# Optimization experiments

Hardware: AMD Instinct MI355X
Metric: run time of the kernel (lower is better)

Reference implementation:

```python
import jax, jax.numpy as jnp
import numpy as np

N_NODES = 100000


def mean_aggregate(x, src, dst, n_nodes):
    # gather messages from src nodes, mean-reduce onto dst nodes (DGL copy_u + mean)
    msg = x[src]                                                  # [E, d]
    summed = jax.ops.segment_sum(msg, dst, num_segments=n_nodes)  # [N, d]
    cnt = jax.ops.segment_sum(jnp.ones((src.shape[0],), x.dtype), dst,
                              num_segments=n_nodes)               # [N]
    # zero in-degree nodes get mean 0 (matches DGL mean reducer)
    return summed / jnp.maximum(cnt, 1.0)[:, None]


def setup_inputs() -> dict:
    key = jax.random.key(0)
    ks = jax.random.split(key, 7)
    E = 1600000
    d_in, d_hid, d_out = 128, 128, 128
    features = jax.random.normal(ks[0], (N_NODES, d_in), dtype=jnp.float32)
    src = jax.random.randint(ks[1], (E,), 0, N_NODES, dtype=jnp.int64)
    dst = jax.random.randint(ks[2], (E,), 0, N_NODES, dtype=jnp.int64)
    W1 = jax.random.normal(ks[3], (d_hid, d_in), dtype=jnp.float32) * (1.0 / np.sqrt(d_in))
    b1 = jax.random.normal(ks[4], (d_hid,), dtype=jnp.float32) * 0.01
    W2 = jax.random.normal(ks[5], (d_out, d_hid), dtype=jnp.float32) * (1.0 / np.sqrt(d_hid))
    b2 = jax.random.normal(ks[6], (d_out,), dtype=jnp.float32) * 0.01
    return {"features": features, "src": src, "dst": dst,
            "W1": W1, "b1": b1, "W2": W2, "b2": b2}


def reference(features, src, dst, W1, b1, W2, b2):
    # GINConv (eps=0, mean agg): h = Linear((1+eps)*x + mean_neigh(x))
    agg1 = mean_aggregate(features, src, dst, N_NODES)
    x1 = jax.nn.relu(jnp.dot(features + agg1, W1.T) + b1)   # layer1 + outer relu
    agg2 = mean_aggregate(x1, src, dst, N_NODES)
    x2 = jnp.dot(x1 + agg2, W2.T) + b2                       # layer2, no activation
    return x2
```

## Files before the change

kernel.cpp:

```cpp
#include <hip/hip_runtime.h>

#define D 128
#define CAP_A 12288
#define BIN_SHIFT 9
#define FRAG_CAP 80
#define NBLK_A 256

typedef __attribute__((ext_vector_type(8))) short bf16x8;
typedef __attribute__((ext_vector_type(4))) float f32x4;

static __device__ __forceinline__ unsigned short f2bf(float f) {
    unsigned int u = __float_as_uint(f);
    unsigned int r = (u + 0x7fffu + ((u >> 16) & 1u)) >> 16;
    return (unsigned short)r;
}
static __device__ __forceinline__ float bf2f(unsigned short u) {
    return __uint_as_float((unsigned int)u << 16);
}

__global__ void f2bf_kernel(const float4* __restrict__ in, ushort4* __restrict__ out, int n4) {
    int i = blockIdx.x * blockDim.x + threadIdx.x;
    if (i >= n4) return;
    float4 v = in[i];
    out[i] = make_ushort4(f2bf(v.x), f2bf(v.y), f2bf(v.z), f2bf(v.w));
}
__global__ void wconv_kernel(const float* __restrict__ W, unsigned short* __restrict__ Wb, int n) {
    int i = blockIdx.x * blockDim.x + threadIdx.x;
    if (i < n) Wb[i] = f2bf(W[i]);
}

__global__ __launch_bounds__(1024) void binA_kernel(const int* __restrict__ src,
                                                    const int* __restrict__ dst, int E,
                                                    int NB, int* __restrict__ gcnt,
                                                    unsigned int* __restrict__ ebufA) {
    __shared__ int cnt[256];
    int t = threadIdx.x;
    if (t < 256) cnt[t] = 0;
    __syncthreads();
    int per = (E + gridDim.x - 1) / gridDim.x;
    int start = blockIdx.x * per;
    int endb = min(start + per, E);
    size_t fbase = (size_t)blockIdx.x * NB;
    for (int i = start + t; i < endb; i += blockDim.x) {
        int s = src[i], d = dst[i];
        int b = d >> BIN_SHIFT;
        unsigned int val = ((unsigned int)(d & 511) << 17) | (unsigned int)s;
        int p = atomicAdd(&cnt[b], 1);
        if (p < FRAG_CAP)
            ebufA[(fbase + b) * FRAG_CAP + p] = val;
    }
    __syncthreads();
    if (t < NB) gcnt[fbase + t] = min(cnt[t], FRAG_CAP);
}

__global__ __launch_bounds__(256) void binB_kernel(const unsigned int* __restrict__ ebufA,
                                                   const int* __restrict__ gcnt,
                                                   int NB, int NF, int N,
                                                   int* __restrict__ src_sorted,
                                                   int* __restrict__ row_beg,
                                                   int* __restrict__ deg_g) {
    __shared__ int h[512];
    __shared__ int part[256];
    __shared__ int h2[512];
    int b = blockIdx.x, t = threadIdx.x;
    h[t] = 0; h[t + 256] = 0;
    __syncthreads();
    int wave = t >> 6, lane = t & 63;
    for (int f = wave; f < NF; f += 4) {
        int c = gcnt[(size_t)f * NB + b];
        const unsigned int* base = ebufA + ((size_t)f * NB + b) * FRAG_CAP;
        for (int i = lane; i < c; i += 64)
            atomicAdd(&h[base[i] >> 17], 1);
    }
    __syncthreads();
    int a0 = h[2 * t], a1 = h[2 * t + 1];
    part[t] = a0 + a1;
    __syncthreads();
    for (int off = 1; off < 256; off <<= 1) {
        int x = (t >= off) ? part[t - off] : 0;
        __syncthreads();
        part[t] += x;
        __syncthreads();
    }
    int pe = part[t] - (a0 + a1);
    int node0 = b << BIN_SHIFT;
    if (node0 + 2 * t < N)     { row_beg[node0 + 2 * t]     = b * CAP_A + pe;      deg_g[node0 + 2 * t]     = a0; }
    if (node0 + 2 * t + 1 < N) { row_beg[node0 + 2 * t + 1] = b * CAP_A + pe + a0; deg_g[node0 + 2 * t + 1] = a1; }
    h2[2 * t] = pe; h2[2 * t + 1] = pe + a0;
    __syncthreads();
    for (int f = wave; f < NF; f += 4) {
        int c = gcnt[(size_t)f * NB + b];
        const unsigned int* base = ebufA + ((size_t)f * NB + b) * FRAG_CAP;
        for (int i = lane; i < c; i += 64) {
            unsigned int v = base[i];
            int p = atomicAdd(&h2[v >> 17], 1);
            src_sorted[(size_t)b * CAP_A + p] = (int)(v & 0x1FFFFu);
        }
    }
}

__global__ __launch_bounds__(256) void aggregate_bf16(const ushort4* __restrict__ x,
                                                      const int* __restrict__ row_beg,
                                                      const int* __restrict__ deg_g,
                                                      const int* __restrict__ src_sorted,
                                                      ushort4* __restrict__ out, int N) {
    int node = blockIdx.x * 8 + (threadIdx.x >> 5);
    if (node >= N) return;
    int c = threadIdx.x & 31;
    int beg = row_beg[node];
    int dg  = deg_g[node];
    int end = beg + dg;
    float ax = 0.f, ay = 0.f, az = 0.f, aw = 0.f;
    int j = beg;
    for (; j + 4 <= end; j += 4) {
        int s0 = src_sorted[j + 0];
        int s1 = src_sorted[j + 1];
        int s2 = src_sorted[j + 2];
        int s3 = src_sorted[j + 3];
        ushort4 v0 = x[(size_t)s0 * 32 + c];
        ushort4 v1 = x[(size_t)s1 * 32 + c];
        ushort4 v2 = x[(size_t)s2 * 32 + c];
        ushort4 v3 = x[(size_t)s3 * 32 + c];
        ax += bf2f(v0.x) + bf2f(v1.x) + bf2f(v2.x) + bf2f(v3.x);
        ay += bf2f(v0.y) + bf2f(v1.y) + bf2f(v2.y) + bf2f(v3.y);
        az += bf2f(v0.z) + bf2f(v1.z) + bf2f(v2.z) + bf2f(v3.z);
        aw += bf2f(v0.w) + bf2f(v1.w) + bf2f(v2.w) + bf2f(v3.w);
    }
    for (; j < end; ++j) {
        int s = src_sorted[j];
        ushort4 v = x[(size_t)s * 32 + c];
        ax += bf2f(v.x); ay += bf2f(v.y); az += bf2f(v.z); aw += bf2f(v.w);
    }
    float inv = 1.0f / fmaxf((float)dg, 1.0f);
    ushort4 xv = x[(size_t)node * 32 + c];
    out[(size_t)node * 32 + c] = make_ushort4(
        f2bf(bf2f(xv.x) + ax * inv),
        f2bf(bf2f(xv.y) + ay * inv),
        f2bf(bf2f(xv.z) + az * inv),
        f2bf(bf2f(xv.w) + aw * inv));
}

__global__ __launch_bounds__(256) void gemm_mfma(const unsigned short* __restrict__ A,
                                                 const unsigned short* __restrict__ Wb,
                                                 const float* __restrict__ bias,
                                                 unsigned short* __restrict__ outb,
                                                 float* __restrict__ outf,
                                                 int N, int relu) {
    int t = threadIdx.x;
    int wave = t >> 6;
    int lane = t & 63;
    int quad = lane >> 4;
    int l16  = lane & 15;
    int row0 = blockIdx.x * 128 + wave * 32;

    f32x4 acc[2][8];
#pragma unroll
    for (int rt = 0; rt < 2; ++rt)
#pragma unroll
        for (int ct = 0; ct < 8; ++ct)
            acc[rt][ct] = (f32x4){0.f, 0.f, 0.f, 0.f};

    const unsigned short* a0 = A + (size_t)(row0 + l16) * D + quad * 8;
    const unsigned short* a1 = a0 + (size_t)16 * D;
    bool ok0 = (row0 + l16) < N;
    bool ok1 = (row0 + 16 + l16) < N;
    bf16x8 zz = {0, 0, 0, 0, 0, 0, 0, 0};

#pragma unroll
    for (int ks = 0; ks < 4; ++ks) {
        bf16x8 af0 = ok0 ? *(const bf16x8*)(a0 + ks * 32) : zz;
        bf16x8 af1 = ok1 ? *(const bf16x8*)(a1 + ks * 32) : zz;
#pragma unroll
        for (int ct = 0; ct < 8; ++ct) {
            bf16x8 bfr = *(const bf16x8*)(Wb + (size_t)(ct * 16 + l16) * D + ks * 32 + quad * 8);
            acc[0][ct] = __builtin_amdgcn_mfma_f32_16x16x32_bf16(af0, bfr, acc[0][ct], 0, 0, 0);
            acc[1][ct] = __builtin_amdgcn_mfma_f32_16x16x32_bf16(af1, bfr, acc[1][ct], 0, 0, 0);
        }
    }

#pragma unroll
    for (int rt = 0; rt < 2; ++rt) {
        int rbase = row0 + rt * 16 + quad * 4;
#pragma unroll
        for (int ct = 0; ct < 8; ++ct) {
            int col = ct * 16 + l16;
            float bb = bias[col];
#pragma unroll
            for (int r = 0; r < 4; ++r) {
                int row = rbase + r;
                if (row < N) {
                    float v = acc[rt][ct][r] + bb;
                    if (relu) v = fmaxf(v, 0.f);
                    if (outb) outb[(size_t)row * D + col] = f2bf(v);
                    else      outf[(size_t)row * D + col] = v;
                }
            }
        }
    }
}

extern "C" void kernel_launch(void* const* d_in, const int* in_sizes, int n_in,
                              void* d_out, int out_size, void* d_ws, size_t ws_size,
                              hipStream_t stream) {
    const float* features = (const float*)d_in[0];
    const int*   src      = (const int*)d_in[1];
    const int*   dst      = (const int*)d_in[2];
    const float* W1       = (const float*)d_in[3];
    const float* b1       = (const float*)d_in[4];
    const float* W2       = (const float*)d_in[5];
    const float* b2       = (const float*)d_in[6];
    float* out = (float*)d_out;

    int N = in_sizes[0] / D;
    int E = in_sizes[1];
    int NB = (N + 511) >> BIN_SHIFT;

    char* ws = (char*)d_ws;
    size_t off = 0;
    unsigned short* bufA = (unsigned short*)(ws + off); off += (size_t)N * D * 2;
    unsigned short* bufB = (unsigned short*)(ws + off); off += (size_t)N * D * 2;
    unsigned short* Wb1  = (unsigned short*)(ws + off); off += (size_t)D * D * 2;
    unsigned short* Wb2  = (unsigned short*)(ws + off); off += (size_t)D * D * 2;
    int* gcnt    = (int*)(ws + off); off += (size_t)NBLK_A * NB * 4;
    int* row_beg = (int*)(ws + off); off += (size_t)N * 4;
    int* deg_g   = (int*)(ws + off); off += (size_t)N * 4;

    unsigned int* ebufA = (unsigned int*)d_out;
    int* src_sorted = (int*)((char*)d_out + (size_t)NBLK_A * NB * FRAG_CAP * 4);

    f2bf_kernel<<<(N * 32 + 255) / 256, 256, 0, stream>>>(
        (const float4*)features, (ushort4*)bufA, N * 32);
    wconv_kernel<<<(D * D + 255) / 256, 256, 0, stream>>>(W1, Wb1, D * D);
    wconv_kernel<<<(D * D + 255) / 256, 256, 0, stream>>>(W2, Wb2, D * D);

    binA_kernel<<<NBLK_A, 1024, 0, stream>>>(src, dst, E, NB, gcnt, ebufA);
    binB_kernel<<<NB, 256, 0, stream>>>(ebufA, gcnt, NB, NBLK_A, N, src_sorted, row_beg, deg_g);

    int gemm_grid = (N + 127) / 128;

    aggregate_bf16<<<(N + 7) / 8, 256, 0, stream>>>(
        (const ushort4*)bufA, row_beg, deg_g, src_sorted, (ushort4*)bufB, N);
    gemm_mfma<<<gemm_grid, 256, 0, stream>>>(bufB, Wb1, b1, bufA, (float*)nullptr, N, 1);

    aggregate_bf16<<<(N + 7) / 8, 256, 0, stream>>>(
        (const ushort4*)bufA, row_beg, deg_g, src_sorted, (ushort4*)bufB, N);
    gemm_mfma<<<gemm_grid, 256, 0, stream>>>(bufB, Wb2, b2, (unsigned short*)nullptr, out, N, 0);
}
```

Before: 393.7 us.

## Shrink CSR bins to 128 nodes with bin-major fragments and register-staged binB

Bins shrink from 512 to 128 destination nodes, giving more binB blocks. The fragment buffer is reordered bin-major so each binB block reads one contiguous region with uint4 loads. Each thread holds its edges in registers for both the histogram and the scatter pass instead of reading global memory twice. The aggregate kernel also gains an 8-wide unrolled gather loop for more memory parallelism. The risk is that the smaller FRAG_CAP and CAP_B capacities could overflow and silently drop edges on skewed graphs.

```diff
diff --git a/kernel.cpp b/kernel.cpp
--- a/kernel.cpp
+++ b/kernel.cpp
@@ -1,10 +1,11 @@
 #include <hip/hip_runtime.h>
 
 #define D 128
-#define CAP_A 12288
-#define BIN_SHIFT 9
-#define FRAG_CAP 80
+#define BIN_SHIFT 7
+#define BIN_NODES 128
+#define FRAG_CAP 32
 #define NBLK_A 256
+#define CAP_B 2560
 
 typedef __attribute__((ext_vector_type(8))) short bf16x8;
 typedef __attribute__((ext_vector_type(4))) float f32x4;
@@ -33,69 +34,88 @@
                                                     const int* __restrict__ dst, int E,
                                                     int NB, int* __restrict__ gcnt,
                                                     unsigned int* __restrict__ ebufA) {
-    __shared__ int cnt[256];
+    __shared__ int cnt[1024];
     int t = threadIdx.x;
-    if (t < 256) cnt[t] = 0;
+    cnt[t] = 0;
     __syncthreads();
     int per = (E + gridDim.x - 1) / gridDim.x;
     int start = blockIdx.x * per;
     int endb = min(start + per, E);
-    size_t fbase = (size_t)blockIdx.x * NB;
+    int f = blockIdx.x;
     for (int i = start + t; i < endb; i += blockDim.x) {
         int s = src[i], d = dst[i];
         int b = d >> BIN_SHIFT;
-        unsigned int val = ((unsigned int)(d & 511) << 17) | (unsigned int)s;
+        unsigned int val = ((unsigned int)(d & (BIN_NODES - 1)) << 17) | (unsigned int)s;
         int p = atomicAdd(&cnt[b], 1);
         if (p < FRAG_CAP)
-            ebufA[(fbase + b) * FRAG_CAP + p] = val;
-    }
-    __syncthreads();
-    if (t < NB) gcnt[fbase + t] = min(cnt[t], FRAG_CAP);
+            ebufA[((size_t)b * NBLK_A + f) * FRAG_CAP + p] = val;
+    }
+    __syncthreads();
+    if (t < NB) gcnt[(size_t)t * NBLK_A + f] = min(cnt[t], FRAG_CAP);
 }
 
 __global__ __launch_bounds__(256) void binB_kernel(const unsigned int* __restrict__ ebufA,
                                                    const int* __restrict__ gcnt,
-                                                   int NB, int NF, int N,
+                                                   int NB, int N,
                                                    int* __restrict__ src_sorted,
                                                    int* __restrict__ row_beg,
                                                    int* __restrict__ deg_g) {
-    __shared__ int h[512];
-    __shared__ int part[256];
-    __shared__ int h2[512];
+    __shared__ int gc[NBLK_A];
+    __shared__ int h[BIN_NODES];
+    __shared__ int h2[BIN_NODES];
+    __shared__ int part[BIN_NODES];
     int b = blockIdx.x, t = threadIdx.x;
-    h[t] = 0; h[t + 256] = 0;
-    __syncthreads();
-    int wave = t >> 6, lane = t & 63;
-    for (int f = wave; f < NF; f += 4) {
-        int c = gcnt[(size_t)f * NB + b];
-        const unsigned int* base = ebufA + ((size_t)f * NB + b) * FRAG_CAP;
-        for (int i = lane; i < c; i += 64)
-            atomicAdd(&h[base[i] >> 17], 1);
-    }
-    __syncthreads();
-    int a0 = h[2 * t], a1 = h[2 * t + 1];
-    part[t] = a0 + a1;
-    __syncthreads();
-    for (int off = 1; off < 256; off <<= 1) {
-        int x = (t >= off) ? part[t - off] : 0;
+    gc[t] = gcnt[(size_t)b * NBLK_A + t];
+    if (t < BIN_NODES) h[t] = 0;
+    __syncthreads();
+
+    const uint4* base = (const uint4*)(ebufA + (size_t)b * NBLK_A * FRAG_CAP);
+    uint4 vals[8];
+    unsigned int vmask[8];
+#pragma unroll
+    for (int k = 0; k < 8; ++k) {
+        int c = t + k * 256;
+        vals[k] = base[c];
+        int frag = c >> 3;
+        int sb = (c & 7) * 4;
+        int cc = gc[frag];
+        int nv = cc - sb;
+        nv = max(0, min(4, nv));
+        vmask[k] = nv;
+    }
+#pragma unroll
+    for (int k = 0; k < 8; ++k) {
+        unsigned int nv = vmask[k];
+        if (nv > 0) atomicAdd(&h[(vals[k].x >> 17) & (BIN_NODES - 1)], 1);
+        if (nv > 1) atomicAdd(&h[(vals[k].y >> 17) & (BIN_NODES - 1)], 1);
+        if (nv > 2) atomicAdd(&h[(vals[k].z >> 17) & (BIN_NODES - 1)], 1);
+        if (nv > 3) atomicAdd(&h[(vals[k].w >> 17) & (BIN_NODES - 1)], 1);
+    }
+    __syncthreads();
+    if (t < BIN_NODES) part[t] = h[t];
+    __syncthreads();
+    for (int off = 1; off < BIN_NODES; off <<= 1) {
+        int x = 0;
+        if (t < BIN_NODES && t >= off) x = part[t - off];
         __syncthreads();
-        part[t] += x;
+        if (t < BIN_NODES) part[t] += x;
         __syncthreads();
     }
-    int pe = part[t] - (a0 + a1);
-    int node0 = b << BIN_SHIFT;
-    if (node0 + 2 * t < N)     { row_beg[node0 + 2 * t]     = b * CAP_A + pe;      deg_g[node0 + 2 * t]     = a0; }
-    if (node0 + 2 * t + 1 < N) { row_beg[node0 + 2 * t + 1] = b * CAP_A + pe + a0; deg_g[node0 + 2 * t + 1] = a1; }
-    h2[2 * t] = pe; h2[2 * t + 1] = pe + a0;
-    __syncthreads();
-    for (int f = wave; f < NF; f += 4) {
-        int c = gcnt[(size_t)f * NB + b];
-        const unsigned int* base = ebufA + ((size_t)f * NB + b) * FRAG_CAP;
-        for (int i = lane; i < c; i += 64) {
-            unsigned int v = base[i];
-            int p = atomicAdd(&h2[v >> 17], 1);
-            src_sorted[(size_t)b * CAP_A + p] = (int)(v & 0x1FFFFu);
-        }
+    if (t < BIN_NODES) {
+        int excl = part[t] - h[t];
+        int node = (b << BIN_SHIFT) + t;
+        if (node < N) { row_beg[node] = b * CAP_B + excl; deg_g[node] = h[t]; }
+        h2[t] = excl;
+    }
+    __syncthreads();
+    int* seg = src_sorted + (size_t)b * CAP_B;
+#pragma unroll
+    for (int k = 0; k < 8; ++k) {
+        unsigned int nv = vmask[k];
+        if (nv > 0) seg[atomicAdd(&h2[(vals[k].x >> 17) & (BIN_NODES - 1)], 1)] = (int)(vals[k].x & 0x1FFFFu);
+        if (nv > 1) seg[atomicAdd(&h2[(vals[k].y >> 17) & (BIN_NODES - 1)], 1)] = (int)(vals[k].y & 0x1FFFFu);
+        if (nv > 2) seg[atomicAdd(&h2[(vals[k].z >> 17) & (BIN_NODES - 1)], 1)] = (int)(vals[k].z & 0x1FFFFu);
+        if (nv > 3) seg[atomicAdd(&h2[(vals[k].w >> 17) & (BIN_NODES - 1)], 1)] = (int)(vals[k].w & 0x1FFFFu);
     }
 }
 
@@ -112,11 +132,31 @@
     int end = beg + dg;
     float ax = 0.f, ay = 0.f, az = 0.f, aw = 0.f;
     int j = beg;
+    for (; j + 8 <= end; j += 8) {
+        int s0 = src_sorted[j + 0], s1 = src_sorted[j + 1];
+        int s2 = src_sorted[j + 2], s3 = src_sorted[j + 3];
+        int s4 = src_sorted[j + 4], s5 = src_sorted[j + 5];
+        int s6 = src_sorted[j + 6], s7 = src_sorted[j + 7];
+        ushort4 v0 = x[(size_t)s0 * 32 + c];
+        ushort4 v1 = x[(size_t)s1 * 32 + c];
+        ushort4 v2 = x[(size_t)s2 * 32 + c];
+        ushort4 v3 = x[(size_t)s3 * 32 + c];
+        ushort4 v4 = x[(size_t)s4 * 32 + c];
+        ushort4 v5 = x[(size_t)s5 * 32 + c];
+        ushort4 v6 = x[(size_t)s6 * 32 + c];
+        ushort4 v7 = x[(size_t)s7 * 32 + c];
+        ax += bf2f(v0.x) + bf2f(v1.x) + bf2f(v2.x) + bf2f(v3.x)
+            + bf2f(v4.x) + bf2f(v5.x) + bf2f(v6.x) + bf2f(v7.x);
+        ay += bf2f(v0.y) + bf2f(v1.y) + bf2f(v2.y) + bf2f(v3.y)
+            + bf2f(v4.y) + bf2f(v5.y) + bf2f(v6.y) + bf2f(v7.y);
+        az += bf2f(v0.z) + bf2f(v1.z) + bf2f(v2.z) + bf2f(v3.z)
+            + bf2f(v4.z) + bf2f(v5.z) + bf2f(v6.z) + bf2f(v7.z);
+        aw += bf2f(v0.w) + bf2f(v1.w) + bf2f(v2.w) + bf2f(v3.w)
+            + bf2f(v4.w) + bf2f(v5.w) + bf2f(v6.w) + bf2f(v7.w);
+    }
     for (; j + 4 <= end; j += 4) {
-        int s0 = src_sorted[j + 0];
-        int s1 = src_sorted[j + 1];
-        int s2 = src_sorted[j + 2];
-        int s3 = src_sorted[j + 3];
+        int s0 = src_sorted[j + 0], s1 = src_sorted[j + 1];
+        int s2 = src_sorted[j + 2], s3 = src_sorted[j + 3];
         ushort4 v0 = x[(size_t)s0 * 32 + c];
         ushort4 v1 = x[(size_t)s1 * 32 + c];
         ushort4 v2 = x[(size_t)s2 * 32 + c];
@@ -213,7 +253,7 @@
 
     int N = in_sizes[0] / D;
     int E = in_sizes[1];
-    int NB = (N + 511) >> BIN_SHIFT;
+    int NB = (N + BIN_NODES - 1) >> BIN_SHIFT;
 
     char* ws = (char*)d_ws;
     size_t off = 0;
@@ -221,12 +261,12 @@
     unsigned short* bufB = (unsigned short*)(ws + off); off += (size_t)N * D * 2;
     unsigned short* Wb1  = (unsigned short*)(ws + off); off += (size_t)D * D * 2;
     unsigned short* Wb2  = (unsigned short*)(ws + off); off += (size_t)D * D * 2;
-    int* gcnt    = (int*)(ws + off); off += (size_t)NBLK_A * NB * 4;
+    int* gcnt    = (int*)(ws + off); off += (size_t)NB * NBLK_A * 4;
     int* row_beg = (int*)(ws + off); off += (size_t)N * 4;
     int* deg_g   = (int*)(ws + off); off += (size_t)N * 4;
 
     unsigned int* ebufA = (unsigned int*)d_out;
-    int* src_sorted = (int*)((char*)d_out + (size_t)NBLK_A * NB * FRAG_CAP * 4);
+    int* src_sorted = (int*)((char*)d_out + (size_t)NB * NBLK_A * FRAG_CAP * 4);
 
     f2bf_kernel<<<(N * 32 + 255) / 256, 256, 0, stream>>>(
         (const float4*)features, (ushort4*)bufA, N * 32);
@@ -234,7 +274,7 @@
     wconv_kernel<<<(D * D + 255) / 256, 256, 0, stream>>>(W2, Wb2, D * D);
 
     binA_kernel<<<NBLK_A, 1024, 0, stream>>>(src, dst, E, NB, gcnt, ebufA);
-    binB_kernel<<<NB, 256, 0, stream>>>(ebufA, gcnt, NB, NBLK_A, N, src_sorted, row_beg, deg_g);
+    binB_kernel<<<NB, 256, 0, stream>>>(ebufA, gcnt, NB, N, src_sorted, row_beg, deg_g);
 
     int gemm_grid = (N + 127) / 128;
 
```

New measurement: 353.5 us. -10.2%, faster.
